# Kernel optimization log

Measured on AMD Instinct MI355X. Metric: run time of the kernel, lower is better.

## Reference

```python
import jax, jax.numpy as jnp
import numpy as np

B, S, K, N, GROUP = 4, 8, 4096, 11008, 128
NUM_GROUPS = K // GROUP  # 32


def setup_inputs() -> dict:
    key = jax.random.key(0)
    k1, k2, k3 = jax.random.split(key, 3)
    x = jax.random.normal(k1, (B, S, K), dtype=jnp.float16)
    # packed int4 weights: each byte holds two nibbles (low nibble = even k, high = odd k)
    weight_packed = jax.random.randint(k2, (N, K // 2), 0, 256, dtype=jnp.int32)
    # scales: abs(randn)*0.1 in fp16, as in the torch module
    scales = (jnp.abs(jax.random.normal(k3, (N, NUM_GROUPS), dtype=jnp.float16)) * jnp.float16(0.1))
    return {"x": x, "weight_packed": weight_packed, "scales": scales}


def _dequant(weight_packed, scales, Kd):
    # unpack: low nibble -> even index k, high nibble -> odd index k+1
    n = weight_packed.shape[0]
    low = weight_packed & 0xF
    high = (weight_packed >> 4) & 0xF
    w = jnp.stack([low, high], axis=-1).reshape(n, Kd)  # [N, K] int in [0,16)
    g = Kd // scales.shape[1]
    # group-wise dequant: scale * (w - 8), scale applied in fp32 (matches fp32-accum kernel)
    wq = (w.astype(jnp.float32) - 8.0).reshape(n, scales.shape[1], g)
    wdeq = wq * scales.astype(jnp.float32)[:, :, None]
    return wdeq.reshape(n, Kd)  # [N, K] fp32


def reference(x, weight_packed, scales):
    b, s, kd = x.shape
    wdeq = _dequant(weight_packed, scales, kd)           # [N, K]
    x2 = x.reshape(-1, kd).astype(jnp.float32)           # [M, K], fp32 accumulation
    out = jnp.einsum('mk,nk->mn', x2, wdeq)              # [M, N]
    return out.astype(jnp.float16).reshape(b, s, -1)
```

## Files before the change

kernel.cpp:

```cpp
#include <hip/hip_runtime.h>

#define M 32
#define N 11008
#define K 4096
#define NGROUPS 32
#define BN 16
#define KSPLIT 4
#define KRANGE (K / KSPLIT)
#define BK 256
#define NCHUNK (KRANGE / BK)

typedef _Float16 half8 __attribute__((ext_vector_type(8)));
typedef _Float16 half4 __attribute__((ext_vector_type(4)));
typedef float floatx4 __attribute__((ext_vector_type(4)));

#define WPAIR 260
#define XPAIR 520

__device__ inline void gll16(const void* g, void* l) {
    __builtin_amdgcn_global_load_lds(
        (const __attribute__((address_space(1))) unsigned int*)g,
        (__attribute__((address_space(3))) unsigned int*)l, 16, 0, 0);
}

__global__ __launch_bounds__(512) void xcvt_kernel(
    const float* __restrict__ x, _Float16* __restrict__ xf)
{
    int i = (blockIdx.x * 512 + threadIdx.x) * 4;
    float4 v = *(const float4*)(x + i);
    half4 h;
    h[0] = (_Float16)v.x; h[1] = (_Float16)v.y;
    h[2] = (_Float16)v.z; h[3] = (_Float16)v.w;
    *(half4*)(xf + i) = h;
}

__global__ __launch_bounds__(256) void int4_gemm_kernel(
    const _Float16* __restrict__ xf,
    const int* __restrict__ wp,
    const float* __restrict__ scales,
    float* __restrict__ out)
{
    __shared__ int wsh[8 * WPAIR];
    __shared__ _Float16 xs[16 * XPAIR];

    const int t    = threadIdx.x;
    const int lane = t & 63;
    const int w    = t >> 6;
    const int n0   = blockIdx.x * BN;
    const int ks   = blockIdx.y;
    const int row  = lane & 15;
    const int quad = lane >> 4;

    floatx4 acc0 = {0.f, 0.f, 0.f, 0.f};
    floatx4 acc1 = {0.f, 0.f, 0.f, 0.f};

    const half8 c1032 = (half8)(_Float16)1032.0f;

    for (int c = 0; c < NCHUNK; ++c) {
        const int kc = ks * KRANGE + c * BK;

        #pragma unroll
        for (int i = 0; i < 2; ++i) {
            int p = w * 2 + i;
            int r = 2 * p + (lane >> 5);
            const int* g = wp + (long)(n0 + r) * (K / 2) + (kc >> 1) + (lane & 31) * 4;
            gll16(g, &wsh[p * WPAIR]);
        }
        #pragma unroll
        for (int i = 0; i < 4; ++i) {
            int p = w * 4 + i;
            int m = 2 * p + (lane >> 5);
            const _Float16* g = xf + m * K + kc + (lane & 31) * 8;
            gll16(g, &xs[p * XPAIR]);
        }
        __syncthreads();

        const float s = scales[(n0 + row) * NGROUPS + (kc >> 7) + (w >> 1)];
        floatx4 t0 = {0.f, 0.f, 0.f, 0.f};
        floatx4 t1 = {0.f, 0.f, 0.f, 0.f};
        #pragma unroll
        for (int kk = 0; kk < 2; ++kk) {
            const int kl = w * 64 + kk * 32;
            int4 wv = *(const int4*)&wsh[(row >> 1) * WPAIR + (row & 1) * 128 + (kl >> 1) + quad * 4];
            uint4 uw;
            {
                unsigned int b;
                b = (unsigned int)wv.x;
                uw.x = ((b | (b << 12)) & 0x000F000Fu) | 0x64006400u;
                b = (unsigned int)wv.y;
                uw.y = ((b | (b << 12)) & 0x000F000Fu) | 0x64006400u;
                b = (unsigned int)wv.z;
                uw.z = ((b | (b << 12)) & 0x000F000Fu) | 0x64006400u;
                b = (unsigned int)wv.w;
                uw.w = ((b | (b << 12)) & 0x000F000Fu) | 0x64006400u;
            }
            half8 bfrag = __builtin_bit_cast(half8, uw) - c1032;

            int x0 = (row >> 1) * XPAIR + (row & 1) * 256 + kl + quad * 8;
            half8 a0 = *(const half8*)&xs[x0];
            half8 a1 = *(const half8*)&xs[x0 + 8 * XPAIR];
            t0 = __builtin_amdgcn_mfma_f32_16x16x32_f16(a0, bfrag, t0, 0, 0, 0);
            t1 = __builtin_amdgcn_mfma_f32_16x16x32_f16(a1, bfrag, t1, 0, 0, 0);
        }
        #pragma unroll
        for (int r = 0; r < 4; ++r) {
            acc0[r] += s * t0[r];
            acc1[r] += s * t1[r];
        }
        __syncthreads();
    }

    float* red = (float*)xs;
    #pragma unroll
    for (int r = 0; r < 4; ++r) {
        red[w * 512 + (quad * 4 + r) * 16 + row]      = acc0[r];
        red[w * 512 + (quad * 4 + r + 16) * 16 + row] = acc1[r];
    }
    __syncthreads();
    #pragma unroll
    for (int i = 0; i < 2; ++i) {
        int o = t + 256 * i;
        float sum = red[o] + red[512 + o] + red[1024 + o] + red[1536 + o];
        int m = o >> 4;
        int n = o & 15;
        atomicAdd(&out[m * N + n0 + n], sum);
    }
}

extern "C" void kernel_launch(void* const* d_in, const int* in_sizes, int n_in,
                              void* d_out, int out_size, void* d_ws, size_t ws_size,
                              hipStream_t stream) {
    const float* x      = (const float*)d_in[0];
    const int* wp       = (const int*)d_in[1];
    const float* scales = (const float*)d_in[2];
    float* out          = (float*)d_out;
    _Float16* xf16      = (_Float16*)d_ws;

    hipMemsetAsync(out, 0, (size_t)M * N * sizeof(float), stream);
    xcvt_kernel<<<dim3((M * K) / (512 * 4)), 512, 0, stream>>>(x, xf16);
    int4_gemm_kernel<<<dim3(N / BN, KSPLIT), 256, 0, stream>>>(xf16, wp, scales, out);
}
```

Measured before the change: 141.5 us.

## Drop LDS staging and x-convert kernel; load operands directly into registers

```diff
diff --git a/kernel.cpp b/kernel.cpp
--- a/kernel.cpp
+++ b/kernel.cpp
@@ -7,41 +7,20 @@
 #define BN 16
 #define KSPLIT 4
 #define KRANGE (K / KSPLIT)
-#define BK 256
-#define NCHUNK (KRANGE / BK)
+#define KWAVE (KRANGE / 4)
+#define NSTEP (KWAVE / 32)
 
 typedef _Float16 half8 __attribute__((ext_vector_type(8)));
-typedef _Float16 half4 __attribute__((ext_vector_type(4)));
 typedef float floatx4 __attribute__((ext_vector_type(4)));
-
-#define WPAIR 260
-#define XPAIR 520
-
-__device__ inline void gll16(const void* g, void* l) {
-    __builtin_amdgcn_global_load_lds(
-        (const __attribute__((address_space(1))) unsigned int*)g,
-        (__attribute__((address_space(3))) unsigned int*)l, 16, 0, 0);
-}
-
-__global__ __launch_bounds__(512) void xcvt_kernel(
-    const float* __restrict__ x, _Float16* __restrict__ xf)
-{
-    int i = (blockIdx.x * 512 + threadIdx.x) * 4;
-    float4 v = *(const float4*)(x + i);
-    half4 h;
-    h[0] = (_Float16)v.x; h[1] = (_Float16)v.y;
-    h[2] = (_Float16)v.z; h[3] = (_Float16)v.w;
-    *(half4*)(xf + i) = h;
-}
+typedef float float8 __attribute__((ext_vector_type(8)));
 
 __global__ __launch_bounds__(256) void int4_gemm_kernel(
-    const _Float16* __restrict__ xf,
+    const float* __restrict__ x,
     const int* __restrict__ wp,
     const float* __restrict__ scales,
     float* __restrict__ out)
 {
-    __shared__ int wsh[8 * WPAIR];
-    __shared__ _Float16 xs[16 * XPAIR];
+    __shared__ float red[4 * 512];
 
     const int t    = threadIdx.x;
     const int lane = t & 63;
@@ -51,66 +30,61 @@
     const int row  = lane & 15;
     const int quad = lane >> 4;
 
+    const int kbase = ks * KRANGE + w * KWAVE;
+
+    const int*   gw = wp + (long)(n0 + row) * (K / 2) + (kbase >> 1) + quad * 4;
+    const float* gx = x  + (long)row * K + kbase + quad * 8;
+
+    int4 wv[NSTEP];
+    #pragma unroll
+    for (int s = 0; s < NSTEP; ++s)
+        wv[s] = *(const int4*)(gw + s * 16);
+
+    const float s0 = scales[(n0 + row) * NGROUPS + ks * 8 + w * 2 + 0];
+    const float s1 = scales[(n0 + row) * NGROUPS + ks * 8 + w * 2 + 1];
+
     floatx4 acc0 = {0.f, 0.f, 0.f, 0.f};
     floatx4 acc1 = {0.f, 0.f, 0.f, 0.f};
-
     const half8 c1032 = (half8)(_Float16)1032.0f;
 
-    for (int c = 0; c < NCHUNK; ++c) {
-        const int kc = ks * KRANGE + c * BK;
-
-        #pragma unroll
-        for (int i = 0; i < 2; ++i) {
-            int p = w * 2 + i;
-            int r = 2 * p + (lane >> 5);
-            const int* g = wp + (long)(n0 + r) * (K / 2) + (kc >> 1) + (lane & 31) * 4;
-            gll16(g, &wsh[p * WPAIR]);
-        }
-        #pragma unroll
-        for (int i = 0; i < 4; ++i) {
-            int p = w * 4 + i;
-            int m = 2 * p + (lane >> 5);
-            const _Float16* g = xf + m * K + kc + (lane & 31) * 8;
-            gll16(g, &xs[p * XPAIR]);
-        }
-        __syncthreads();
-
-        const float s = scales[(n0 + row) * NGROUPS + (kc >> 7) + (w >> 1)];
+    #pragma unroll
+    for (int g = 0; g < 2; ++g) {
         floatx4 t0 = {0.f, 0.f, 0.f, 0.f};
         floatx4 t1 = {0.f, 0.f, 0.f, 0.f};
         #pragma unroll
-        for (int kk = 0; kk < 2; ++kk) {
-            const int kl = w * 64 + kk * 32;
-            int4 wv = *(const int4*)&wsh[(row >> 1) * WPAIR + (row & 1) * 128 + (kl >> 1) + quad * 4];
+        for (int si = 0; si < 4; ++si) {
+            const int s = g * 4 + si;
+            float8 xa = *(const float8*)(gx + (long)s * 32);
+            float8 xb = *(const float8*)(gx + 16 * K + (long)s * 32);
+            half8 a0, a1;
+            #pragma unroll
+            for (int j = 0; j < 8; ++j) {
+                a0[j] = (_Float16)xa[j];
+                a1[j] = (_Float16)xb[j];
+            }
             uint4 uw;
-            {
-                unsigned int b;
-                b = (unsigned int)wv.x;
-                uw.x = ((b | (b << 12)) & 0x000F000Fu) | 0x64006400u;
-                b = (unsigned int)wv.y;
-                uw.y = ((b | (b << 12)) & 0x000F000Fu) | 0x64006400u;
-                b = (unsigned int)wv.z;
-                uw.z = ((b | (b << 12)) & 0x000F000Fu) | 0x64006400u;
-                b = (unsigned int)wv.w;
-                uw.w = ((b | (b << 12)) & 0x000F000Fu) | 0x64006400u;
-            }
-            half8 bfrag = __builtin_bit_cast(half8, uw) - c1032;
+            unsigned int b;
+            b = (unsigned int)wv[s].x;
+            uw.x = ((b | (b << 12)) & 0x000F000Fu) | 0x64006400u;
+            b = (unsigned int)wv[s].y;
+            uw.y = ((b | (b << 12)) & 0x000F000Fu) | 0x64006400u;
+            b = (unsigned int)wv[s].z;
+            uw.z = ((b | (b << 12)) & 0x000F000Fu) | 0x64006400u;
+            b = (unsigned int)wv[s].w;
+            uw.w = ((b | (b << 12)) & 0x000F000Fu) | 0x64006400u;
+            half8 bf = __builtin_bit_cast(half8, uw) - c1032;
 
-            int x0 = (row >> 1) * XPAIR + (row & 1) * 256 + kl + quad * 8;
-            half8 a0 = *(const half8*)&xs[x0];
-            half8 a1 = *(const half8*)&xs[x0 + 8 * XPAIR];
-            t0 = __builtin_amdgcn_mfma_f32_16x16x32_f16(a0, bfrag, t0, 0, 0, 0);
-            t1 = __builtin_amdgcn_mfma_f32_16x16x32_f16(a1, bfrag, t1, 0, 0, 0);
+            t0 = __builtin_amdgcn_mfma_f32_16x16x32_f16(a0, bf, t0, 0, 0, 0);
+            t1 = __builtin_amdgcn_mfma_f32_16x16x32_f16(a1, bf, t1, 0, 0, 0);
         }
+        const float sg = g ? s1 : s0;
         #pragma unroll
         for (int r = 0; r < 4; ++r) {
-            acc0[r] += s * t0[r];
-            acc1[r] += s * t1[r];
+            acc0[r] += sg * t0[r];
+            acc1[r] += sg * t1[r];
         }
-        __syncthreads();
     }
 
-    float* red = (float*)xs;
     #pragma unroll
     for (int r = 0; r < 4; ++r) {
         red[w * 512 + (quad * 4 + r) * 16 + row]      = acc0[r];
@@ -119,10 +93,10 @@
     __syncthreads();
     #pragma unroll
     for (int i = 0; i < 2; ++i) {
-        int o = t + 256 * i;
-        float sum = red[o] + red[512 + o] + red[1024 + o] + red[1536 + o];
-        int m = o >> 4;
-        int n = o & 15;
+        const int o = t + 256 * i;
+        const float sum = red[o] + red[512 + o] + red[1024 + o] + red[1536 + o];
+        const int m = o >> 4;
+        const int n = o & 15;
         atomicAdd(&out[m * N + n0 + n], sum);
     }
 }
@@ -134,9 +108,7 @@
     const int* wp       = (const int*)d_in[1];
     const float* scales = (const float*)d_in[2];
     float* out          = (float*)d_out;
-    _Float16* xf16      = (_Float16*)d_ws;
 
     hipMemsetAsync(out, 0, (size_t)M * N * sizeof(float), stream);
-    xcvt_kernel<<<dim3((M * K) / (512 * 4)), 512, 0, stream>>>(x, xf16);
-    int4_gemm_kernel<<<dim3(N / BN, KSPLIT), 256, 0, stream>>>(xf16, wp, scales, out);
+    int4_gemm_kernel<<<dim3(N / BN, KSPLIT), 256, 0, stream>>>(x, wp, scales, out);
 }
```

New measurement: 167.8 us. +18.6%, slower.

## Fuse fp32-to-fp16 activation conversion into GEMM and double N tile

Applied to the files above, without the earlier changes.

```diff
diff --git a/kernel.cpp b/kernel.cpp
--- a/kernel.cpp
+++ b/kernel.cpp
@@ -4,18 +4,19 @@
 #define N 11008
 #define K 4096
 #define NGROUPS 32
-#define BN 16
+#define BN 32
 #define KSPLIT 4
 #define KRANGE (K / KSPLIT)
 #define BK 256
 #define NCHUNK (KRANGE / BK)
+#define WPAIR 260
+#define RSTRIDE 36
+#define RWAVE (32 * RSTRIDE)
 
 typedef _Float16 half8 __attribute__((ext_vector_type(8)));
-typedef _Float16 half4 __attribute__((ext_vector_type(4)));
+typedef _Float16 half2v __attribute__((ext_vector_type(2)));
 typedef float floatx4 __attribute__((ext_vector_type(4)));
-
-#define WPAIR 260
-#define XPAIR 520
+typedef float float8 __attribute__((ext_vector_type(8)));
 
 __device__ inline void gll16(const void* g, void* l) {
     __builtin_amdgcn_global_load_lds(
@@ -23,25 +24,34 @@
         (__attribute__((address_space(3))) unsigned int*)l, 16, 0, 0);
 }
 
-__global__ __launch_bounds__(512) void xcvt_kernel(
-    const float* __restrict__ x, _Float16* __restrict__ xf)
-{
-    int i = (blockIdx.x * 512 + threadIdx.x) * 4;
-    float4 v = *(const float4*)(x + i);
-    half4 h;
-    h[0] = (_Float16)v.x; h[1] = (_Float16)v.y;
-    h[2] = (_Float16)v.z; h[3] = (_Float16)v.w;
-    *(half4*)(xf + i) = h;
+__device__ inline half8 cvt8(float8 v) {
+    half8 r; half2v p;
+    p = __builtin_bit_cast(half2v, __builtin_amdgcn_cvt_pkrtz(v[0], v[1])); r[0] = p[0]; r[1] = p[1];
+    p = __builtin_bit_cast(half2v, __builtin_amdgcn_cvt_pkrtz(v[2], v[3])); r[2] = p[0]; r[3] = p[1];
+    p = __builtin_bit_cast(half2v, __builtin_amdgcn_cvt_pkrtz(v[4], v[5])); r[4] = p[0]; r[5] = p[1];
+    p = __builtin_bit_cast(half2v, __builtin_amdgcn_cvt_pkrtz(v[6], v[7])); r[6] = p[0]; r[7] = p[1];
+    return r;
+}
+
+__device__ inline half8 unpack8(int4 wv) {
+    uint4 uw; unsigned int b;
+    b = (unsigned)wv.x; uw.x = ((b | (b << 12)) & 0x000F000Fu) | 0x64006400u;
+    b = (unsigned)wv.y; uw.y = ((b | (b << 12)) & 0x000F000Fu) | 0x64006400u;
+    b = (unsigned)wv.z; uw.z = ((b | (b << 12)) & 0x000F000Fu) | 0x64006400u;
+    b = (unsigned)wv.w; uw.w = ((b | (b << 12)) & 0x000F000Fu) | 0x64006400u;
+    const half8 c1032 = (half8)(_Float16)1032.0f;
+    return __builtin_bit_cast(half8, uw) - c1032;
 }
 
 __global__ __launch_bounds__(256) void int4_gemm_kernel(
-    const _Float16* __restrict__ xf,
+    const float* __restrict__ x,
     const int* __restrict__ wp,
     const float* __restrict__ scales,
     float* __restrict__ out)
 {
-    __shared__ int wsh[8 * WPAIR];
-    __shared__ _Float16 xs[16 * XPAIR];
+    __shared__ int lds[4 * RWAVE];
+    int*   wsh = lds;
+    float* red = (float*)lds;
 
     const int t    = threadIdx.x;
     const int lane = t & 63;
@@ -51,78 +61,76 @@
     const int row  = lane & 15;
     const int quad = lane >> 4;
 
-    floatx4 acc0 = {0.f, 0.f, 0.f, 0.f};
-    floatx4 acc1 = {0.f, 0.f, 0.f, 0.f};
+    floatx4 acc00 = {0,0,0,0}, acc01 = {0,0,0,0};
+    floatx4 acc10 = {0,0,0,0}, acc11 = {0,0,0,0};
 
-    const half8 c1032 = (half8)(_Float16)1032.0f;
+    const float* gx0 = x + (long)row * K + ks * KRANGE + quad * 8;
+    const float* gx1 = gx0 + 16 * K;
+    const int woff = w * 64;
 
     for (int c = 0; c < NCHUNK; ++c) {
         const int kc = ks * KRANGE + c * BK;
 
         #pragma unroll
-        for (int i = 0; i < 2; ++i) {
-            int p = w * 2 + i;
-            int r = 2 * p + (lane >> 5);
-            const int* g = wp + (long)(n0 + r) * (K / 2) + (kc >> 1) + (lane & 31) * 4;
-            gll16(g, &wsh[p * WPAIR]);
-        }
-        #pragma unroll
         for (int i = 0; i < 4; ++i) {
             int p = w * 4 + i;
-            int m = 2 * p + (lane >> 5);
-            const _Float16* g = xf + m * K + kc + (lane & 31) * 8;
-            gll16(g, &xs[p * XPAIR]);
+            int r = 2 * p + (lane >> 5);
+            const int* gsrc = wp + (long)(n0 + r) * (K / 2) + (kc >> 1) + (lane & 31) * 4;
+            gll16(gsrc, &wsh[p * WPAIR]);
         }
+        float8 xa0 = *(const float8*)(gx0 + c * BK + woff);
+        float8 xb0 = *(const float8*)(gx1 + c * BK + woff);
+        float8 xa1 = *(const float8*)(gx0 + c * BK + woff + 32);
+        float8 xb1 = *(const float8*)(gx1 + c * BK + woff + 32);
+        const int grp = (kc >> 7) + (w >> 1);
+        const float sA = scales[(n0 + row) * NGROUPS + grp];
+        const float sB = scales[(n0 + 16 + row) * NGROUPS + grp];
+        half8 a00 = cvt8(xa0), a10 = cvt8(xb0);
+        half8 a01 = cvt8(xa1), a11 = cvt8(xb1);
         __syncthreads();
 
-        const float s = scales[(n0 + row) * NGROUPS + (kc >> 7) + (w >> 1)];
-        floatx4 t0 = {0.f, 0.f, 0.f, 0.f};
-        floatx4 t1 = {0.f, 0.f, 0.f, 0.f};
+        floatx4 t00 = {0,0,0,0}, t01 = {0,0,0,0};
+        floatx4 t10 = {0,0,0,0}, t11 = {0,0,0,0};
         #pragma unroll
         for (int kk = 0; kk < 2; ++kk) {
-            const int kl = w * 64 + kk * 32;
-            int4 wv = *(const int4*)&wsh[(row >> 1) * WPAIR + (row & 1) * 128 + (kl >> 1) + quad * 4];
-            uint4 uw;
-            {
-                unsigned int b;
-                b = (unsigned int)wv.x;
-                uw.x = ((b | (b << 12)) & 0x000F000Fu) | 0x64006400u;
-                b = (unsigned int)wv.y;
-                uw.y = ((b | (b << 12)) & 0x000F000Fu) | 0x64006400u;
-                b = (unsigned int)wv.z;
-                uw.z = ((b | (b << 12)) & 0x000F000Fu) | 0x64006400u;
-                b = (unsigned int)wv.w;
-                uw.w = ((b | (b << 12)) & 0x000F000Fu) | 0x64006400u;
-            }
-            half8 bfrag = __builtin_bit_cast(half8, uw) - c1032;
-
-            int x0 = (row >> 1) * XPAIR + (row & 1) * 256 + kl + quad * 8;
-            half8 a0 = *(const half8*)&xs[x0];
-            half8 a1 = *(const half8*)&xs[x0 + 8 * XPAIR];
-            t0 = __builtin_amdgcn_mfma_f32_16x16x32_f16(a0, bfrag, t0, 0, 0, 0);
-            t1 = __builtin_amdgcn_mfma_f32_16x16x32_f16(a1, bfrag, t1, 0, 0, 0);
+            const int kl = woff + kk * 32;
+            const int bidx = (row >> 1) * WPAIR + (row & 1) * 128 + (kl >> 1) + quad * 4;
+            half8 b0 = unpack8(*(const int4*)&wsh[bidx]);
+            half8 b1 = unpack8(*(const int4*)&wsh[bidx + 8 * WPAIR]);
+            half8 a0 = kk ? a01 : a00;
+            half8 a1 = kk ? a11 : a10;
+            t00 = __builtin_amdgcn_mfma_f32_16x16x32_f16(a0, b0, t00, 0, 0, 0);
+            t01 = __builtin_amdgcn_mfma_f32_16x16x32_f16(a0, b1, t01, 0, 0, 0);
+            t10 = __builtin_amdgcn_mfma_f32_16x16x32_f16(a1, b0, t10, 0, 0, 0);
+            t11 = __builtin_amdgcn_mfma_f32_16x16x32_f16(a1, b1, t11, 0, 0, 0);
         }
         #pragma unroll
         for (int r = 0; r < 4; ++r) {
-            acc0[r] += s * t0[r];
-            acc1[r] += s * t1[r];
+            acc00[r] += sA * t00[r];
+            acc01[r] += sB * t01[r];
+            acc10[r] += sA * t10[r];
+            acc11[r] += sB * t11[r];
         }
         __syncthreads();
     }
 
-    float* red = (float*)xs;
+    float* rw = red + w * RWAVE;
     #pragma unroll
     for (int r = 0; r < 4; ++r) {
-        red[w * 512 + (quad * 4 + r) * 16 + row]      = acc0[r];
-        red[w * 512 + (quad * 4 + r + 16) * 16 + row] = acc1[r];
+        const int m0 = quad * 4 + r;
+        rw[m0 * RSTRIDE + row]             = acc00[r];
+        rw[m0 * RSTRIDE + 16 + row]        = acc01[r];
+        rw[(m0 + 16) * RSTRIDE + row]      = acc10[r];
+        rw[(m0 + 16) * RSTRIDE + 16 + row] = acc11[r];
     }
     __syncthreads();
     #pragma unroll
-    for (int i = 0; i < 2; ++i) {
-        int o = t + 256 * i;
-        float sum = red[o] + red[512 + o] + red[1024 + o] + red[1536 + o];
-        int m = o >> 4;
-        int n = o & 15;
+    for (int i = 0; i < 4; ++i) {
+        const int o = t + 256 * i;
+        const int m = o >> 5;
+        const int n = o & 31;
+        const int a = m * RSTRIDE + n;
+        const float sum = red[a] + red[RWAVE + a] + red[2 * RWAVE + a] + red[3 * RWAVE + a];
         atomicAdd(&out[m * N + n0 + n], sum);
     }
 }
@@ -134,9 +142,7 @@
     const int* wp       = (const int*)d_in[1];
     const float* scales = (const float*)d_in[2];
     float* out          = (float*)d_out;
-    _Float16* xf16      = (_Float16*)d_ws;
 
-    hipMemsetAsync(out, 0, (size_t)M * N * sizeof(float), stream);
-    xcvt_kernel<<<dim3((M * K) / (512 * 4)), 512, 0, stream>>>(x, xf16);
-    int4_gemm_kernel<<<dim3(N / BN, KSPLIT), 256, 0, stream>>>(xf16, wp, scales, out);
+    (void)hipMemsetAsync(out, 0, (size_t)M * N * sizeof(float), stream);
+    int4_gemm_kernel<<<dim3(N / BN, KSPLIT), 256, 0, stream>>>(x, wp, scales, out);
 }
```

New measurement: 151.3 us. 1.07x slower.

## Give each wave a private 4-deep LDS pipeline and drop block barriers

Applied to the files above, without the earlier changes.

```diff
diff --git a/kernel.cpp b/kernel.cpp
--- a/kernel.cpp
+++ b/kernel.cpp
@@ -5,22 +5,33 @@
 #define K 4096
 #define NGROUPS 32
 #define BN 16
-#define KSPLIT 4
+#define KSPLIT 2
 #define KRANGE (K / KSPLIT)
-#define BK 256
-#define NCHUNK (KRANGE / BK)
+#define KWAVE (KRANGE / 4)
+#define DEPTH 4
+#define WSLOT 256
+#define XSLOT 512
+#define LWAVE (DEPTH * (WSLOT + XSLOT))
+#define RS 17
 
 typedef _Float16 half8 __attribute__((ext_vector_type(8)));
 typedef _Float16 half4 __attribute__((ext_vector_type(4)));
 typedef float floatx4 __attribute__((ext_vector_type(4)));
 
-#define WPAIR 260
-#define XPAIR 520
-
 __device__ inline void gll16(const void* g, void* l) {
     __builtin_amdgcn_global_load_lds(
         (const __attribute__((address_space(1))) unsigned int*)g,
         (__attribute__((address_space(3))) unsigned int*)l, 16, 0, 0);
+}
+
+__device__ inline half8 unpack8(int4 wv) {
+    uint4 uw; unsigned int b;
+    b = (unsigned)wv.x; uw.x = ((b | (b << 12)) & 0x000F000Fu) | 0x64006400u;
+    b = (unsigned)wv.y; uw.y = ((b | (b << 12)) & 0x000F000Fu) | 0x64006400u;
+    b = (unsigned)wv.z; uw.z = ((b | (b << 12)) & 0x000F000Fu) | 0x64006400u;
+    b = (unsigned)wv.w; uw.w = ((b | (b << 12)) & 0x000F000Fu) | 0x64006400u;
+    const half8 c1032 = (half8)(_Float16)1032.0f;
+    return __builtin_bit_cast(half8, uw) - c1032;
 }
 
 __global__ __launch_bounds__(512) void xcvt_kernel(
@@ -34,14 +45,43 @@
     *(half4*)(xf + i) = h;
 }
 
+
+#define WAITV(n) asm volatile("s_waitcnt vmcnt(" #n ")" ::: "memory")
+#define SB() __builtin_amdgcn_sched_barrier(0)
+
+#define ISSUE(s) {                                                  \
+    gll16(gw  + (s) * 16, wbase + ((s) & 3) * WSLOT);               \
+    gll16(gx0 + (s) * 32, xbase + ((s) & 3) * XSLOT);               \
+    gll16(gx1 + (s) * 32, xbase + ((s) & 3) * XSLOT + 256);         \
+}
+
+#define COMPUTE(s) {                                                \
+    int4 wv  = *(const int4*)&wbase[((s) & 3) * WSLOT + lane4];     \
+    half8 a0 = *(const half8*)&xh[((s) & 3) * 1024 + lane8];        \
+    half8 a1 = *(const half8*)&xh[((s) & 3) * 1024 + 512 + lane8];  \
+    SB();                                                           \
+    half8 b = unpack8(wv);                                          \
+    t0 = __builtin_amdgcn_mfma_f32_16x16x32_f16(a0, b, t0, 0, 0, 0);\
+    t1 = __builtin_amdgcn_mfma_f32_16x16x32_f16(a1, b, t1, 0, 0, 0);\
+}
+
+#define APPLY(sg) {                                                 \
+    _Pragma("unroll")                                               \
+    for (int r = 0; r < 4; ++r) {                                   \
+        acc0[r] += (sg) * t0[r];                                    \
+        acc1[r] += (sg) * t1[r];                                    \
+    }                                                               \
+    t0 = (floatx4){0.f,0.f,0.f,0.f};                                \
+    t1 = (floatx4){0.f,0.f,0.f,0.f};                                \
+}
+
 __global__ __launch_bounds__(256) void int4_gemm_kernel(
     const _Float16* __restrict__ xf,
     const int* __restrict__ wp,
     const float* __restrict__ scales,
     float* __restrict__ out)
 {
-    __shared__ int wsh[8 * WPAIR];
-    __shared__ _Float16 xs[16 * XPAIR];
+    __shared__ int lds[4 * LWAVE];
 
     const int t    = threadIdx.x;
     const int lane = t & 63;
@@ -50,80 +90,61 @@
     const int ks   = blockIdx.y;
     const int row  = lane & 15;
     const int quad = lane >> 4;
+    const int lane4 = lane * 4;
+    const int lane8 = lane * 8;
 
-    floatx4 acc0 = {0.f, 0.f, 0.f, 0.f};
-    floatx4 acc1 = {0.f, 0.f, 0.f, 0.f};
+    const int kw = ks * KRANGE + w * KWAVE;
 
-    const half8 c1032 = (half8)(_Float16)1032.0f;
+    int* wbase = &lds[w * LWAVE];
+    int* xbase = wbase + DEPTH * WSLOT;
+    const _Float16* xh = (const _Float16*)xbase;
 
-    for (int c = 0; c < NCHUNK; ++c) {
-        const int kc = ks * KRANGE + c * BK;
+    const int*      gw  = wp + (long)(n0 + row) * (K / 2) + (kw >> 1) + quad * 4;
+    const _Float16* gx0 = xf + (long)row * K + kw + quad * 8;
+    const _Float16* gx1 = gx0 + 16 * K;
 
-        #pragma unroll
-        for (int i = 0; i < 2; ++i) {
-            int p = w * 2 + i;
-            int r = 2 * p + (lane >> 5);
-            const int* g = wp + (long)(n0 + r) * (K / 2) + (kc >> 1) + (lane & 31) * 4;
-            gll16(g, &wsh[p * WPAIR]);
-        }
-        #pragma unroll
-        for (int i = 0; i < 4; ++i) {
-            int p = w * 4 + i;
-            int m = 2 * p + (lane >> 5);
-            const _Float16* g = xf + m * K + kc + (lane & 31) * 8;
-            gll16(g, &xs[p * XPAIR]);
-        }
-        __syncthreads();
+    const float* sp = scales + (long)(n0 + row) * NGROUPS + (kw >> 7);
+    const float sg0 = sp[0], sg1 = sp[1], sg2 = sp[2], sg3 = sp[3];
 
-        const float s = scales[(n0 + row) * NGROUPS + (kc >> 7) + (w >> 1)];
-        floatx4 t0 = {0.f, 0.f, 0.f, 0.f};
-        floatx4 t1 = {0.f, 0.f, 0.f, 0.f};
-        #pragma unroll
-        for (int kk = 0; kk < 2; ++kk) {
-            const int kl = w * 64 + kk * 32;
-            int4 wv = *(const int4*)&wsh[(row >> 1) * WPAIR + (row & 1) * 128 + (kl >> 1) + quad * 4];
-            uint4 uw;
-            {
-                unsigned int b;
-                b = (unsigned int)wv.x;
-                uw.x = ((b | (b << 12)) & 0x000F000Fu) | 0x64006400u;
-                b = (unsigned int)wv.y;
-                uw.y = ((b | (b << 12)) & 0x000F000Fu) | 0x64006400u;
-                b = (unsigned int)wv.z;
-                uw.z = ((b | (b << 12)) & 0x000F000Fu) | 0x64006400u;
-                b = (unsigned int)wv.w;
-                uw.w = ((b | (b << 12)) & 0x000F000Fu) | 0x64006400u;
-            }
-            half8 bfrag = __builtin_bit_cast(half8, uw) - c1032;
+    floatx4 acc0 = {0,0,0,0}, acc1 = {0,0,0,0};
+    floatx4 t0   = {0,0,0,0}, t1   = {0,0,0,0};
 
-            int x0 = (row >> 1) * XPAIR + (row & 1) * 256 + kl + quad * 8;
-            half8 a0 = *(const half8*)&xs[x0];
-            half8 a1 = *(const half8*)&xs[x0 + 8 * XPAIR];
-            t0 = __builtin_amdgcn_mfma_f32_16x16x32_f16(a0, bfrag, t0, 0, 0, 0);
-            t1 = __builtin_amdgcn_mfma_f32_16x16x32_f16(a1, bfrag, t1, 0, 0, 0);
-        }
-        #pragma unroll
-        for (int r = 0; r < 4; ++r) {
-            acc0[r] += s * t0[r];
-            acc1[r] += s * t1[r];
-        }
-        __syncthreads();
-    }
+    ISSUE(0) ISSUE(1) ISSUE(2) ISSUE(3)
 
-    float* red = (float*)xs;
+    WAITV(9); COMPUTE(0)              SB(); ISSUE(4)
+    WAITV(9); COMPUTE(1)              SB(); ISSUE(5)
+    WAITV(9); COMPUTE(2)              SB(); ISSUE(6)
+    WAITV(9); COMPUTE(3)  APPLY(sg0) SB(); ISSUE(7)
+    WAITV(9); COMPUTE(4)              SB(); ISSUE(8)
+    WAITV(9); COMPUTE(5)              SB(); ISSUE(9)
+    WAITV(9); COMPUTE(6)              SB(); ISSUE(10)
+    WAITV(9); COMPUTE(7)  APPLY(sg1) SB(); ISSUE(11)
+    WAITV(9); COMPUTE(8)              SB(); ISSUE(12)
+    WAITV(9); COMPUTE(9)              SB(); ISSUE(13)
+    WAITV(9); COMPUTE(10)             SB(); ISSUE(14)
+    WAITV(9); COMPUTE(11) APPLY(sg2) SB(); ISSUE(15)
+    WAITV(9); COMPUTE(12)
+    WAITV(6); COMPUTE(13)
+    WAITV(3); COMPUTE(14)
+    WAITV(0); COMPUTE(15) APPLY(sg3)
+
+    __syncthreads();
+    float* red = (float*)lds;
+    float* rw  = red + w * 32 * RS;
     #pragma unroll
     for (int r = 0; r < 4; ++r) {
-        red[w * 512 + (quad * 4 + r) * 16 + row]      = acc0[r];
-        red[w * 512 + (quad * 4 + r + 16) * 16 + row] = acc1[r];
+        rw[(quad * 4 + r) * RS + row]      = acc0[r];
+        rw[(quad * 4 + r + 16) * RS + row] = acc1[r];
     }
     __syncthreads();
     #pragma unroll
     for (int i = 0; i < 2; ++i) {
-        int o = t + 256 * i;
-        float sum = red[o] + red[512 + o] + red[1024 + o] + red[1536 + o];
-        int m = o >> 4;
-        int n = o & 15;
-        atomicAdd(&out[m * N + n0 + n], sum);
+        const int o = t + 256 * i;
+        const int m = o >> 4;
+        const int n = o & 15;
+        const int a = m * RS + n;
+        const float sum = red[a] + red[32 * RS + a] + red[64 * RS + a] + red[96 * RS + a];
+        atomicAdd(&out[(long)m * N + n0 + n], sum);
     }
 }
 
@@ -136,7 +157,7 @@
     float* out          = (float*)d_out;
     _Float16* xf16      = (_Float16*)d_ws;
 
-    hipMemsetAsync(out, 0, (size_t)M * N * sizeof(float), stream);
+    (void)hipMemsetAsync(out, 0, (size_t)M * N * sizeof(float), stream);
     xcvt_kernel<<<dim3((M * K) / (512 * 4)), 512, 0, stream>>>(x, xf16);
     int4_gemm_kernel<<<dim3(N / BN, KSPLIT), 256, 0, stream>>>(xf16, wp, scales, out);
 }
```

After: 160.7 us. 13.6% more time.
